# Kernel optimization log

Hardware: AMD Instinct MI355X
Metric: run time of the kernel (lower is better)

The kernel has to match this reference:

```python
import jax, jax.numpy as jnp
from jax import lax
import numpy as np

B, T, F, H, L = 64, 2048, 8, 128, 2


def _uniform(key, shape, k):
    return jax.random.uniform(key, shape, jnp.float32, -k, k)


def setup_inputs() -> dict:
    key = jax.random.key(0)
    keys = jax.random.split(key, 12)
    k = 1.0 / np.sqrt(H)
    inp = {"x": jax.random.normal(keys[0], (B, T, F), jnp.float32)}
    # layer 0: input size F; layer 1: input size H (PyTorch nn.LSTM layout: gates i,f,g,o)
    inp["w_ih0"] = _uniform(keys[1], (4 * H, F), k)
    inp["w_hh0"] = _uniform(keys[2], (4 * H, H), k)
    inp["b_ih0"] = _uniform(keys[3], (4 * H,), k)
    inp["b_hh0"] = _uniform(keys[4], (4 * H,), k)
    inp["w_ih1"] = _uniform(keys[5], (4 * H, H), k)
    inp["w_hh1"] = _uniform(keys[6], (4 * H, H), k)
    inp["b_ih1"] = _uniform(keys[7], (4 * H,), k)
    inp["b_hh1"] = _uniform(keys[8], (4 * H,), k)
    inp["w_lin"] = _uniform(keys[9], (F, H), 1.0 / np.sqrt(H))
    inp["b_lin"] = _uniform(keys[10], (F,), 1.0 / np.sqrt(H))
    return inp


def _lstm_layer(x, w_ih, w_hh, b_ih, b_hh):
    # x: [B, T, D_in]; precompute input contribution to gates: [B, T, 4H]
    xg = jnp.einsum('btd,gd->btg', x, w_ih) + b_ih + b_hh
    h0 = jnp.zeros((x.shape[0], w_hh.shape[1]), x.dtype)
    c0 = jnp.zeros_like(h0)

    def step(carry, xg_t):
        h, c = carry
        gates = xg_t + h @ w_hh.T  # [B, 4H]
        i, f, g, o = jnp.split(gates, 4, axis=-1)
        i = jax.nn.sigmoid(i)
        f = jax.nn.sigmoid(f)
        g = jnp.tanh(g)
        o = jax.nn.sigmoid(o)
        c = f * c + i * g
        h = o * jnp.tanh(c)
        return (h, c), h

    _, hs = lax.scan(step, (h0, c0), jnp.swapaxes(xg, 0, 1))  # hs: [T, B, H]
    return jnp.swapaxes(hs, 0, 1)


def reference(x, w_ih0, w_hh0, b_ih0, b_hh0, w_ih1, w_hh1, b_ih1, b_hh1, w_lin, b_lin):
    h = _lstm_layer(x, w_ih0, w_hh0, b_ih0, b_hh0)
    h = _lstm_layer(h, w_ih1, w_hh1, b_ih1, b_hh1)
    return jnp.einsum('bth,fh->btf', h, w_lin) + b_lin
```

## Files before the change

### kernel.cpp

```cpp
#include <hip/hip_runtime.h>

#define B_ 64
#define T_ 2048
#define F_ 8
#define H_ 128
#define RING_LD 68
#define CHUNK 64
#define NCH (T_ / CHUNK)
#define GRING 16
#define H0_DW (CHUNK * 64)
#define H0C_LD 68
#define Z_LD 516

typedef _Float16 v2h   __attribute__((ext_vector_type(2)));
typedef _Float16 f16x8 __attribute__((ext_vector_type(8)));
typedef float    f32x4 __attribute__((ext_vector_type(4)));

__device__ __forceinline__ unsigned pk2h(float lo, float hi) {
    v2h p;
    p[0] = (_Float16)lo;
    p[1] = (_Float16)hi;
    return __builtin_bit_cast(unsigned, p);
}

#if __has_builtin(__builtin_amdgcn_fdot2)
__device__ __forceinline__ float fdot2a(unsigned a, unsigned b, float c) {
    return __builtin_amdgcn_fdot2(__builtin_bit_cast(v2h, a),
                                  __builtin_bit_cast(v2h, b), c, false);
}
#else
__device__ __forceinline__ float fdot2a(unsigned a, unsigned b, float c) {
    v2h av = __builtin_bit_cast(v2h, a);
    v2h bv = __builtin_bit_cast(v2h, b);
    c += (float)av[0] * (float)bv[0];
    c += (float)av[1] * (float)bv[1];
    return c;
}
#endif

__device__ __forceinline__ float sigm(float x) {
    return 1.0f / (1.0f + __expf(-x));
}
__device__ __forceinline__ float tanh_f(float x) {
    float e = __expf(2.0f * x);
    return 1.0f - 2.0f / (e + 1.0f);
}

__device__ __forceinline__ f32x4 mfma16(f16x8 a, f16x8 b, f32x4 c) {
    return __builtin_amdgcn_mfma_f32_16x16x32_f16(a, b, c, 0, 0, 0);
}

#if __has_builtin(__builtin_amdgcn_mov_dpp)
template <int CTRL>
__device__ __forceinline__ float qperm(float v) {
    int i = __builtin_bit_cast(int, v);
    i = __builtin_amdgcn_mov_dpp(i, CTRL, 0xF, 0xF, true);
    return __builtin_bit_cast(float, i);
}
__device__ __forceinline__ float lane_xor1(float v) { return qperm<0xB1>(v); }
__device__ __forceinline__ float lane_xor2(float v) { return qperm<0x4E>(v); }
#else
__device__ __forceinline__ float lane_xor1(float v) {
    int i = __builtin_amdgcn_ds_swizzle(__builtin_bit_cast(int, v), 0x041F);
    return __builtin_bit_cast(float, i);
}
__device__ __forceinline__ float lane_xor2(float v) {
    int i = __builtin_amdgcn_ds_swizzle(__builtin_bit_cast(int, v), 0x081F);
    return __builtin_bit_cast(float, i);
}
#endif

__global__ __launch_bounds__(512, 2)
void lstm2_pc3_kernel(const float* __restrict__ x,
                      const float* __restrict__ wih0,
                      const float* __restrict__ whh0,
                      const float* __restrict__ bih0,
                      const float* __restrict__ bhh0,
                      const float* __restrict__ wih1,
                      const float* __restrict__ whh1,
                      const float* __restrict__ bih1,
                      const float* __restrict__ bhh1,
                      const float* __restrict__ wlin,
                      const float* __restrict__ blin,
                      unsigned* __restrict__ h0g,
                      int* __restrict__ flags,
                      float* __restrict__ out)
{
    __shared__ __align__(16) unsigned arena[25760];
    __shared__ float blin_f[F_];

    const int tid = threadIdx.x;
    int* prog = flags;
    int* done = flags + 64;

    if (blockIdx.x < 64) {
        const int b = blockIdx.x;
        unsigned* x_lds = arena;
        unsigned* ring  = arena + 8192;

        const int h_idx = tid >> 2;
        const int sub   = tid & 3;
        const int growA = (0x3120 >> (sub * 4)) & 0xF;
        const int rowA  = growA * H_ + h_idx;

        const float4* xp = (const float4*)(x + (size_t)b * T_ * F_);
        #pragma unroll
        for (int i = 0; i < 8; ++i) {
            int idx = tid + i * 512;
            float4 v = xp[idx];
            x_lds[idx * 2 + 0] = pk2h(v.x, v.y);
            x_lds[idx * 2 + 1] = pk2h(v.z, v.w);
        }

        unsigned rwih0[4];
        {
            const float4* p = (const float4*)(wih0 + (size_t)rowA * F_);
            float4 v0 = p[0], v1 = p[1];
            rwih0[0] = pk2h(v0.x, v0.y); rwih0[1] = pk2h(v0.z, v0.w);
            rwih0[2] = pk2h(v1.x, v1.y); rwih0[3] = pk2h(v1.z, v1.w);
        }
        unsigned rwhh0[64];
        {
            const float4* p = (const float4*)(whh0 + (size_t)rowA * H_);
            #pragma unroll
            for (int i = 0; i < 32; ++i) {
                float4 v = p[i];
                rwhh0[i * 2 + 0] = pk2h(v.x, v.y);
                rwhh0[i * 2 + 1] = pk2h(v.z, v.w);
            }
        }
        const float bias0 = bih0[rowA] + bhh0[rowA];

        if (tid < 64) ring[63 * 64 + tid] = 0u;
        __syncthreads();

        const bool is_g = (sub == 1);
        const bool lo2  = (sub < 2);
        float c0 = 0.0f;

        for (int t = 0; t < T_; ++t) {
            {
                float aa = bias0, ab = 0.0f, ba = 0.0f, bb = 0.0f;
                uint4 xv = *(const uint4*)&x_lds[t * 4];
                aa = fdot2a(rwih0[0], xv.x, aa);
                ab = fdot2a(rwih0[1], xv.y, ab);
                ba = fdot2a(rwih0[2], xv.z, ba);
                bb = fdot2a(rwih0[3], xv.w, bb);
                const unsigned* hr = &ring[((t + 63) & 63) * 64];
                #pragma unroll
                for (int j = 0; j < 16; ++j) {
                    uint4 hv = *(const uint4*)&hr[j * 4];
                    aa = fdot2a(rwhh0[j * 4 + 0], hv.x, aa);
                    ab = fdot2a(rwhh0[j * 4 + 1], hv.y, ab);
                    ba = fdot2a(rwhh0[j * 4 + 2], hv.z, ba);
                    bb = fdot2a(rwhh0[j * 4 + 3], hv.w, bb);
                }
                float a = (aa + ab) + (ba + bb);
                float xin = is_g ? 2.0f * a : a;
                float s   = sigm(xin);
                float act = is_g ? 2.0f * s - 1.0f : s;
                float s1  = lane_xor1(act);
                float p   = lo2 ? act * s1 : (sub == 2 ? act : s1) * c0;
                float cn  = p + lane_xor2(p);
                c0 = cn;
                float oval = (sub == 2) ? s1 : act;
                float h = oval * tanh_f(cn);
                if (sub == 2) ((_Float16*)&ring[(t & 63) * 64])[h_idx] = (_Float16)h;
            }
            __syncthreads();

            if ((t & 63) == 63) {
                const int c = t >> 6;
                if (c >= GRING) {
                    while (__hip_atomic_load(&done[b], __ATOMIC_ACQUIRE,
                                             __HIP_MEMORY_SCOPE_AGENT) < c - GRING + 1)
                        __builtin_amdgcn_s_sleep(8);
                    __syncthreads();
                }
                unsigned* dst = h0g + ((size_t)b * GRING + (c & (GRING - 1))) * H0_DW;
                uint4 v0 = *(const uint4*)&ring[tid * 8];
                uint4 v1 = *(const uint4*)&ring[tid * 8 + 4];
                *(uint4*)&dst[tid * 8]     = v0;
                *(uint4*)&dst[tid * 8 + 4] = v1;
                __syncthreads();
                if (tid == 0)
                    __hip_atomic_store(&prog[b], c + 1, __ATOMIC_RELEASE,
                                       __HIP_MEMORY_SCOPE_AGENT);
            }
        }
    } else {
        const int b = blockIdx.x - 64;
        unsigned* h0c    = arena;
        unsigned* h1ring = arena + 4352;
        float*    zih1   = (float*)(arena + 8704);
        unsigned* wlin_p = arena + 25216;

        const int w   = tid >> 6;
        const int l   = tid & 63;
        const int n   = l & 15;
        const int grp = l >> 4;

        f16x8 wih1f[4][4], whh1f[4][4];
        #pragma unroll
        for (int j = 0; j < 4; ++j) {
            const int row = j * H_ + w * 16 + n;
            #pragma unroll
            for (int s = 0; s < 4; ++s) {
                const float* p1 = wih1 + (size_t)row * H_ + s * 32 + grp * 8;
                const float* p2 = whh1 + (size_t)row * H_ + s * 32 + grp * 8;
                f16x8 f1, f2;
                #pragma unroll
                for (int jj = 0; jj < 8; ++jj) {
                    f1[jj] = (_Float16)p1[jj];
                    f2[jj] = (_Float16)p2[jj];
                }
                wih1f[j][s] = f1;
                whh1f[j][s] = f2;
            }
        }
        #pragma unroll
        for (int j = 0; j < 4; ++j)
            #pragma unroll
            for (int s = 0; s < 4; ++s) {
                asm("" : "+a"(wih1f[j][s]));
                asm("" : "+a"(whh1f[j][s]));
            }

        float bb1[4];
        #pragma unroll
        for (int j = 0; j < 4; ++j) {
            const int row = j * H_ + w * 16 + n;
            bb1[j] = bih1[row] + bhh1[row];
        }
        {
            float2 v = ((const float2*)wlin)[tid];
            wlin_p[(tid >> 6) * RING_LD + (tid & 63)] = pk2h(v.x, v.y);
        }
        if (tid < F_) blin_f[tid] = blin[tid];
        if (tid < 64) h1ring[63 * RING_LD + tid] = 0u;
        __syncthreads();

        float c1 = 0.0f;
        const f32x4 Z4 = {0.0f, 0.0f, 0.0f, 0.0f};

        for (int c = 0; c < NCH; ++c) {
            while (__hip_atomic_load(&prog[b], __ATOMIC_ACQUIRE,
                                     __HIP_MEMORY_SCOPE_AGENT) < c + 1)
                __builtin_amdgcn_s_sleep(8);
            const unsigned* src = h0g + ((size_t)b * GRING + (c & (GRING - 1))) * H0_DW;
            {
                const int tick = tid >> 3;
                const int off  = (tid & 7) * 8;
                uint4 v0 = *(const uint4*)&src[tick * 64 + off];
                uint4 v1 = *(const uint4*)&src[tick * 64 + off + 4];
                *(uint4*)&h0c[tick * H0C_LD + off]     = v0;
                *(uint4*)&h0c[tick * H0C_LD + off + 4] = v1;
            }
            __syncthreads();
            if (tid == 0)
                __hip_atomic_store(&done[b], c + 1, __ATOMIC_RELAXED,
                                   __HIP_MEMORY_SCOPE_AGENT);

            for (int half = 0; half < 2; ++half) {
                #pragma unroll
                for (int mt = 0; mt < 2; ++mt) {
                    f32x4 d0 = Z4, d1 = Z4, d2 = Z4, d3 = Z4;
                    const int trow = half * 32 + mt * 16 + n;
                    #pragma unroll
                    for (int s = 0; s < 4; ++s) {
                        f16x8 ah = __builtin_bit_cast(
                            f16x8, *(const uint4*)&h0c[trow * H0C_LD + s * 16 + grp * 4]);
                        d0 = mfma16(ah, wih1f[0][s], d0);
                        d1 = mfma16(ah, wih1f[1][s], d1);
                        d2 = mfma16(ah, wih1f[2][s], d2);
                        d3 = mfma16(ah, wih1f[3][s], d3);
                    }
                    const int zr = mt * 16 + grp * 4;
                    #pragma unroll
                    for (int reg = 0; reg < 4; ++reg) {
                        zih1[(zr + reg) * Z_LD + 0 * H_ + w * 16 + n] = d0[reg];
                        zih1[(zr + reg) * Z_LD + 1 * H_ + w * 16 + n] = d1[reg];
                        zih1[(zr + reg) * Z_LD + 2 * H_ + w * 16 + n] = d2[reg];
                        zih1[(zr + reg) * Z_LD + 3 * H_ + w * 16 + n] = d3[reg];
                    }
                }

                for (int tk = 0; tk < 32; ++tk) {
                    const int t  = c * CHUNK + half * 32 + tk;
                    const unsigned* h1r = &h1ring[((t + 63) & 63) * RING_LD];
                    f32x4 a0, a1, a2, a3;
                    {
                        f16x8 ah = __builtin_bit_cast(f16x8, *(const uint4*)&h1r[grp * 4]);
                        a0 = mfma16(ah, whh1f[0][0], Z4);
                        a1 = mfma16(ah, whh1f[1][0], Z4);
                        a2 = mfma16(ah, whh1f[2][0], Z4);
                        a3 = mfma16(ah, whh1f[3][0], Z4);
                    }
                    #pragma unroll
                    for (int s = 1; s < 4; ++s) {
                        f16x8 ah = __builtin_bit_cast(
                            f16x8, *(const uint4*)&h1r[s * 16 + grp * 4]);
                        a0 = mfma16(ah, whh1f[0][s], a0);
                        a1 = mfma16(ah, whh1f[1][s], a1);
                        a2 = mfma16(ah, whh1f[2][s], a2);
                        a3 = mfma16(ah, whh1f[3][s], a3);
                    }
                    const int zbase = (half * 32 + tk) * 0 + tk;
                    const float* zp = &zih1[(half * 32 + tk - half * 32) * Z_LD];
                    float gi = sigm(a0[0] + zp[0 * H_ + w * 16 + n] + bb1[0]);
                    float gf = sigm(a1[0] + zp[1 * H_ + w * 16 + n] + bb1[1]);
                    float gg = tanh_f(a2[0] + zp[2 * H_ + w * 16 + n] + bb1[2]);
                    float go = sigm(a3[0] + zp[3 * H_ + w * 16 + n] + bb1[3]);
                    (void)zbase;
                    c1 = gf * c1 + gi * gg;
                    float hh = go * tanh_f(c1);
                    if (l < 16)
                        ((_Float16*)&h1ring[(t & 63) * RING_LD])[w * 16 + l] = (_Float16)hh;
                    __syncthreads();
                }
            }

            {
                const int tick_i = tid >> 3;
                const int fo     = tid & 7;
                const unsigned* hp = &h1ring[tick_i * RING_LD];
                const unsigned* wv = &wlin_p[fo * RING_LD];
                float a = 0.0f;
                #pragma unroll
                for (int j = 0; j < 16; ++j) {
                    uint4 hv = *(const uint4*)&hp[j * 4];
                    uint4 wq = *(const uint4*)&wv[j * 4];
                    a = fdot2a(wq.x, hv.x, a);
                    a = fdot2a(wq.y, hv.y, a);
                    a = fdot2a(wq.z, hv.z, a);
                    a = fdot2a(wq.w, hv.w, a);
                }
                out[(size_t)b * T_ * F_ + (size_t)c * CHUNK * F_ + tid] = a + blin_f[fo];
            }
        }
    }
}

__global__ __launch_bounds__(512, 2)
void lstm2_burst_kernel(const float* __restrict__ x,
                        const float* __restrict__ wih0,
                        const float* __restrict__ whh0,
                        const float* __restrict__ bih0,
                        const float* __restrict__ bhh0,
                        const float* __restrict__ wih1,
                        const float* __restrict__ whh1,
                        const float* __restrict__ bih1,
                        const float* __restrict__ bhh1,
                        const float* __restrict__ wlin,
                        const float* __restrict__ blin,
                        float* __restrict__ out)
{
    __shared__ __align__(16) unsigned x_lds[T_ * F_ / 2];
    __shared__ __align__(16) unsigned h0_p[2][H_ / 2];
    __shared__ __align__(16) unsigned h1_ring[64 * RING_LD];
    __shared__ __align__(16) unsigned wlin_p[F_ * RING_LD];
    __shared__ float blin_f[F_];

    const int tid   = threadIdx.x;
    const int b     = blockIdx.x;
    const int h_idx = tid >> 2;
    const int sub   = tid & 3;
    const int grow  = (0x3120 >> (sub * 4)) & 0xF;
    const int row   = grow * H_ + h_idx;

    const float4* xp = (const float4*)(x + (size_t)b * T_ * F_);
    #pragma unroll
    for (int i = 0; i < 8; ++i) {
        int idx = tid + i * 512;
        float4 v = xp[idx];
        x_lds[idx * 2 + 0] = pk2h(v.x, v.y);
        x_lds[idx * 2 + 1] = pk2h(v.z, v.w);
    }

    unsigned rwih0[4];
    {
        const float4* p = (const float4*)(wih0 + (size_t)row * F_);
        float4 v0 = p[0], v1 = p[1];
        rwih0[0] = pk2h(v0.x, v0.y); rwih0[1] = pk2h(v0.z, v0.w);
        rwih0[2] = pk2h(v1.x, v1.y); rwih0[3] = pk2h(v1.z, v1.w);
    }
    unsigned rwhh0[64], rwih1[64], rwhh1[64];
    {
        const float4* p = (const float4*)(whh0 + (size_t)row * H_);
        #pragma unroll
        for (int i = 0; i < 32; ++i) {
            float4 v = p[i];
            rwhh0[i * 2 + 0] = pk2h(v.x, v.y);
            rwhh0[i * 2 + 1] = pk2h(v.z, v.w);
        }
    }
    {
        const float4* p = (const float4*)(wih1 + (size_t)row * H_);
        #pragma unroll
        for (int i = 0; i < 32; ++i) {
            float4 v = p[i];
            rwih1[i * 2 + 0] = pk2h(v.x, v.y);
            rwih1[i * 2 + 1] = pk2h(v.z, v.w);
        }
    }
    {
        const float4* p = (const float4*)(whh1 + (size_t)row * H_);
        #pragma unroll
        for (int i = 0; i < 32; ++i) {
            float4 v = p[i];
            rwhh1[i * 2 + 0] = pk2h(v.x, v.y);
            rwhh1[i * 2 + 1] = pk2h(v.z, v.w);
        }
    }
    const float bias0 = bih0[row] + bhh0[row];
    const float bias1 = bih1[row] + bhh1[row];

    {
        int r = tid >> 6, c = tid & 63;
        float2 v = ((const float2*)wlin)[r * 64 + c];
        wlin_p[r * RING_LD + c] = pk2h(v.x, v.y);
    }
    if (tid < F_) blin_f[tid] = blin[tid];
    if (tid < H_ / 2) { h0_p[0][tid] = 0u; h0_p[1][tid] = 0u; }
    if (tid < H_ / 2) h1_ring[63 * RING_LD + tid] = 0u;
    __syncthreads();

    const bool is_g = (sub == 1);
    const bool lo2  = (sub < 2);
    float c0 = 0.0f, c1 = 0.0f;

    for (int t = 0; t < T_; ++t) {
        const int rp = (t + 1) & 1;
        const int wp = t & 1;
        {
            float aa = bias0, ab = 0.0f;
            uint4 xv = *(const uint4*)&x_lds[t * 4];
            aa = fdot2a(rwih0[0], xv.x, aa);
            ab = fdot2a(rwih0[1], xv.y, ab);
            aa = fdot2a(rwih0[2], xv.z, aa);
            ab = fdot2a(rwih0[3], xv.w, ab);
            const unsigned* hr = &h0_p[rp][0];
            #pragma unroll
            for (int j = 0; j < 16; ++j) {
                uint4 hv = *(const uint4*)&hr[j * 4];
                aa = fdot2a(rwhh0[j * 4 + 0], hv.x, aa);
                ab = fdot2a(rwhh0[j * 4 + 1], hv.y, ab);
                aa = fdot2a(rwhh0[j * 4 + 2], hv.z, aa);
                ab = fdot2a(rwhh0[j * 4 + 3], hv.w, ab);
            }
            float a = aa + ab;
            float xin = is_g ? 2.0f * a : a;
            float s   = sigm(xin);
            float act = is_g ? 2.0f * s - 1.0f : s;
            float s1  = lane_xor1(act);
            float p   = lo2 ? act * s1 : (sub == 2 ? act : s1) * c0;
            float cn  = p + lane_xor2(p);
            c0 = cn;
            float oval = (sub == 2) ? s1 : act;
            float h = oval * tanh_f(cn);
            if (sub == 2) ((_Float16*)&h0_p[wp][0])[h_idx] = (_Float16)h;
        }
        __syncthreads();
        {
            float aa = bias1, ab = 0.0f, ba = 0.0f, bb = 0.0f;
            const unsigned* h0r = &h0_p[wp][0];
            const unsigned* h1r = &h1_ring[((t + 63) & 63) * RING_LD];
            #pragma unroll
            for (int j = 0; j < 16; ++j) {
                uint4 hv0 = *(const uint4*)&h0r[j * 4];
                uint4 hv1 = *(const uint4*)&h1r[j * 4];
                aa = fdot2a(rwih1[j * 4 + 0], hv0.x, aa);
                ab = fdot2a(rwih1[j * 4 + 1], hv0.y, ab);
                aa = fdot2a(rwih1[j * 4 + 2], hv0.z, aa);
                ab = fdot2a(rwih1[j * 4 + 3], hv0.w, ab);
                ba = fdot2a(rwhh1[j * 4 + 0], hv1.x, ba);
                bb = fdot2a(rwhh1[j * 4 + 1], hv1.y, bb);
                ba = fdot2a(rwhh1[j * 4 + 2], hv1.z, ba);
                bb = fdot2a(rwhh1[j * 4 + 3], hv1.w, bb);
            }
            float a = (aa + ab) + (ba + bb);
            float xin = is_g ? 2.0f * a : a;
            float s   = sigm(xin);
            float act = is_g ? 2.0f * s - 1.0f : s;
            float s1  = lane_xor1(act);
            float p   = lo2 ? act * s1 : (sub == 2 ? act : s1) * c1;
            float cn  = p + lane_xor2(p);
            c1 = cn;
            float oval = (sub == 2) ? s1 : act;
            float h = oval * tanh_f(cn);
            if (sub == 2)
                ((_Float16*)&h1_ring[(t & 63) * RING_LD])[h_idx] = (_Float16)h;
        }
        __syncthreads();
        if ((t & 63) == 63) {
            const int tick_i = tid >> 3;
            const int fo     = tid & 7;
            const unsigned* hp = &h1_ring[tick_i * RING_LD];
            const unsigned* wv = &wlin_p[fo * RING_LD];
            float a = 0.0f;
            #pragma unroll
            for (int j = 0; j < 16; ++j) {
                uint4 hv = *(const uint4*)&hp[j * 4];
                uint4 wq = *(const uint4*)&wv[j * 4];
                a = fdot2a(wq.x, hv.x, a);
                a = fdot2a(wq.y, hv.y, a);
                a = fdot2a(wq.z, hv.z, a);
                a = fdot2a(wq.w, hv.w, a);
            }
            out[(size_t)b * T_ * F_ + (size_t)(t - 63) * F_ + tid] = a + blin_f[fo];
        }
    }
}

extern "C" void kernel_launch(void* const* d_in, const int* in_sizes, int n_in,
                              void* d_out, int out_size, void* d_ws, size_t ws_size,
                              hipStream_t stream) {
    const float* x    = (const float*)d_in[0];
    const float* wih0 = (const float*)d_in[1];
    const float* whh0 = (const float*)d_in[2];
    const float* bih0 = (const float*)d_in[3];
    const float* bhh0 = (const float*)d_in[4];
    const float* wih1 = (const float*)d_in[5];
    const float* whh1 = (const float*)d_in[6];
    const float* bih1 = (const float*)d_in[7];
    const float* bhh1 = (const float*)d_in[8];
    const float* wlin = (const float*)d_in[9];
    const float* blin = (const float*)d_in[10];
    float* out = (float*)d_out;

    const size_t h0_bytes = (size_t)B_ * GRING * H0_DW * sizeof(unsigned);
    const size_t need = h0_bytes + 512;
    if (d_ws != nullptr && ws_size >= need) {
        unsigned* h0g = (unsigned*)d_ws;
        int* flags = (int*)((char*)d_ws + h0_bytes);
        hipMemsetAsync(flags, 0, 512, stream);
        lstm2_pc3_kernel<<<dim3(128), dim3(512), 0, stream>>>(
            x, wih0, whh0, bih0, bhh0, wih1, whh1, bih1, bhh1, wlin, blin,
            h0g, flags, out);
    } else {
        lstm2_burst_kernel<<<dim3(B_), dim3(512), 0, stream>>>(
            x, wih0, whh0, bih0, bhh0, wih1, whh1, bih1, bhh1, wlin, blin, out);
    }
}
```

Measured before the change: 1.495 ms.

## Move layer-0 LSTM recurrence from fdot2 dot products to MFMA per chunk

The layer-0 producer blocks drop the per-thread fdot2 gate dot products and adopt the layer-1 scheme. W_hh0 is held in f16 MFMA fragments pinned to AGPRs, and the input projection for each 16-step sub-chunk is computed with MFMA into an LDS z0 buffer. The aim is a shorter serial per-step latency on the critical recurrence, which paces the whole pipeline. The cost is four gate MFMAs per step that keep only one output column, plus an extra LDS round trip for the input projections.

```diff
diff --git a/kernel.cpp b/kernel.cpp
--- a/kernel.cpp
+++ b/kernel.cpp
@@ -9,7 +9,6 @@
 #define NCH (T_ / CHUNK)
 #define GRING 16
 #define H0_DW (CHUNK * 64)
-#define H0C_LD 68
 #define Z_LD 516
 
 typedef _Float16 v2h   __attribute__((ext_vector_type(2)));
@@ -71,7 +70,7 @@
 #endif
 
 __global__ __launch_bounds__(512, 2)
-void lstm2_pc3_kernel(const float* __restrict__ x,
+void lstm2_pc5_kernel(const float* __restrict__ x,
                       const float* __restrict__ wih0,
                       const float* __restrict__ whh0,
                       const float* __restrict__ bih0,
@@ -93,15 +92,16 @@
     int* prog = flags;
     int* done = flags + 64;
 
+    const int w   = tid >> 6;
+    const int l   = tid & 63;
+    const int n   = l & 15;
+    const int grp = l >> 4;
+
     if (blockIdx.x < 64) {
         const int b = blockIdx.x;
         unsigned* x_lds = arena;
         unsigned* ring  = arena + 8192;
-
-        const int h_idx = tid >> 2;
-        const int sub   = tid & 3;
-        const int growA = (0x3120 >> (sub * 4)) & 0xF;
-        const int rowA  = growA * H_ + h_idx;
+        float*    z0    = (float*)(arena + 12288);
 
         const float4* xp = (const float4*)(x + (size_t)b * T_ * F_);
         #pragma unroll
@@ -112,79 +112,119 @@
             x_lds[idx * 2 + 1] = pk2h(v.z, v.w);
         }
 
-        unsigned rwih0[4];
-        {
-            const float4* p = (const float4*)(wih0 + (size_t)rowA * F_);
-            float4 v0 = p[0], v1 = p[1];
-            rwih0[0] = pk2h(v0.x, v0.y); rwih0[1] = pk2h(v0.z, v0.w);
-            rwih0[2] = pk2h(v1.x, v1.y); rwih0[3] = pk2h(v1.z, v1.w);
-        }
-        unsigned rwhh0[64];
-        {
-            const float4* p = (const float4*)(whh0 + (size_t)rowA * H_);
-            #pragma unroll
-            for (int i = 0; i < 32; ++i) {
-                float4 v = p[i];
-                rwhh0[i * 2 + 0] = pk2h(v.x, v.y);
-                rwhh0[i * 2 + 1] = pk2h(v.z, v.w);
-            }
-        }
-        const float bias0 = bih0[rowA] + bhh0[rowA];
+        f16x8 whh0f[4][4];
+        #pragma unroll
+        for (int j = 0; j < 4; ++j) {
+            const int row = j * H_ + w * 16 + n;
+            #pragma unroll
+            for (int s = 0; s < 4; ++s) {
+                const float* p0 = whh0 + (size_t)row * H_ + s * 32 + grp * 8;
+                f16x8 f0;
+                #pragma unroll
+                for (int jj = 0; jj < 8; ++jj) f0[jj] = (_Float16)p0[jj];
+                whh0f[j][s] = f0;
+            }
+        }
+        #pragma unroll
+        for (int j = 0; j < 4; ++j)
+            #pragma unroll
+            for (int s = 0; s < 4; ++s)
+                asm("" : "+a"(whh0f[j][s]));
+
+        f16x8 wih0f[4];
+        #pragma unroll
+        for (int j = 0; j < 4; ++j) {
+            f16x8 f0 = {};
+            if (grp == 0) {
+                const float* p = wih0 + (size_t)(j * H_ + w * 16 + n) * F_;
+                #pragma unroll
+                for (int jj = 0; jj < 8; ++jj) f0[jj] = (_Float16)p[jj];
+            }
+            wih0f[j] = f0;
+        }
+
+        float bb0[4];
+        #pragma unroll
+        for (int j = 0; j < 4; ++j) {
+            const int row = j * H_ + w * 16 + n;
+            bb0[j] = bih0[row] + bhh0[row];
+        }
 
         if (tid < 64) ring[63 * 64 + tid] = 0u;
         __syncthreads();
 
-        const bool is_g = (sub == 1);
-        const bool lo2  = (sub < 2);
         float c0 = 0.0f;
-
-        for (int t = 0; t < T_; ++t) {
+        const f32x4 Z4 = {0.0f, 0.0f, 0.0f, 0.0f};
+
+        for (int ch = 0; ch < NCH; ++ch) {
+            for (int q = 0; q < 4; ++q) {
+                {
+                    const int tg = ch * CHUNK + q * 16 + n;
+                    f16x8 ax = (f16x8){};
+                    if (grp == 0)
+                        ax = __builtin_bit_cast(f16x8, *(const uint4*)&x_lds[tg * 4]);
+                    f32x4 d0 = mfma16(ax, wih0f[0], Z4);
+                    f32x4 d1 = mfma16(ax, wih0f[1], Z4);
+                    f32x4 d2 = mfma16(ax, wih0f[2], Z4);
+                    f32x4 d3 = mfma16(ax, wih0f[3], Z4);
+                    #pragma unroll
+                    for (int reg = 0; reg < 4; ++reg) {
+                        const int zr = (grp * 4 + reg) * Z_LD + w * 16 + n;
+                        z0[zr + 0 * H_] = d0[reg];
+                        z0[zr + 1 * H_] = d1[reg];
+                        z0[zr + 2 * H_] = d2[reg];
+                        z0[zr + 3 * H_] = d3[reg];
+                    }
+                }
+
+                for (int tk = 0; tk < 16; ++tk) {
+                    const int t = ch * CHUNK + q * 16 + tk;
+                    const unsigned* hr = &ring[((t + 63) & 63) * 64];
+                    f32x4 a0, a1, a2, a3;
+                    {
+                        f16x8 ah = __builtin_bit_cast(f16x8, *(const uint4*)&hr[grp * 4]);
+                        a0 = mfma16(ah, whh0f[0][0], Z4);
+                        a1 = mfma16(ah, whh0f[1][0], Z4);
+                        a2 = mfma16(ah, whh0f[2][0], Z4);
+                        a3 = mfma16(ah, whh0f[3][0], Z4);
+                    }
+                    #pragma unroll
+                    for (int s = 1; s < 4; ++s) {
+                        f16x8 ah = __builtin_bit_cast(
+                            f16x8, *(const uint4*)&hr[s * 16 + grp * 4]);
+                        a0 = mfma16(ah, whh0f[0][s], a0);
+                        a1 = mfma16(ah, whh0f[1][s], a1);
+                        a2 = mfma16(ah, whh0f[2][s], a2);
+                        a3 = mfma16(ah, whh0f[3][s], a3);
+                    }
+                    const float* zz = &z0[tk * Z_LD + w * 16 + n];
+                    float gi = sigm(a0[0] + zz[0 * H_] + bb0[0]);
+                    float gf = sigm(a1[0] + zz[1 * H_] + bb0[1]);
+                    float gg = tanh_f(a2[0] + zz[2 * H_] + bb0[2]);
+                    float go = sigm(a3[0] + zz[3 * H_] + bb0[3]);
+                    c0 = gf * c0 + gi * gg;
+                    float hh = go * tanh_f(c0);
+                    if (l < 16)
+                        ((_Float16*)&ring[(t & 63) * 64])[w * 16 + l] = (_Float16)hh;
+                    __syncthreads();
+                }
+            }
+
             {
-                float aa = bias0, ab = 0.0f, ba = 0.0f, bb = 0.0f;
-                uint4 xv = *(const uint4*)&x_lds[t * 4];
-                aa = fdot2a(rwih0[0], xv.x, aa);
-                ab = fdot2a(rwih0[1], xv.y, ab);
-                ba = fdot2a(rwih0[2], xv.z, ba);
-                bb = fdot2a(rwih0[3], xv.w, bb);
-                const unsigned* hr = &ring[((t + 63) & 63) * 64];
-                #pragma unroll
-                for (int j = 0; j < 16; ++j) {
-                    uint4 hv = *(const uint4*)&hr[j * 4];
-                    aa = fdot2a(rwhh0[j * 4 + 0], hv.x, aa);
-                    ab = fdot2a(rwhh0[j * 4 + 1], hv.y, ab);
-                    ba = fdot2a(rwhh0[j * 4 + 2], hv.z, ba);
-                    bb = fdot2a(rwhh0[j * 4 + 3], hv.w, bb);
-                }
-                float a = (aa + ab) + (ba + bb);
-                float xin = is_g ? 2.0f * a : a;
-                float s   = sigm(xin);
-                float act = is_g ? 2.0f * s - 1.0f : s;
-                float s1  = lane_xor1(act);
-                float p   = lo2 ? act * s1 : (sub == 2 ? act : s1) * c0;
-                float cn  = p + lane_xor2(p);
-                c0 = cn;
-                float oval = (sub == 2) ? s1 : act;
-                float h = oval * tanh_f(cn);
-                if (sub == 2) ((_Float16*)&ring[(t & 63) * 64])[h_idx] = (_Float16)h;
-            }
-            __syncthreads();
-
-            if ((t & 63) == 63) {
-                const int c = t >> 6;
-                if (c >= GRING) {
+                if (ch >= GRING) {
                     while (__hip_atomic_load(&done[b], __ATOMIC_ACQUIRE,
-                                             __HIP_MEMORY_SCOPE_AGENT) < c - GRING + 1)
+                                             __HIP_MEMORY_SCOPE_AGENT) < ch - GRING + 1)
                         __builtin_amdgcn_s_sleep(8);
                     __syncthreads();
                 }
-                unsigned* dst = h0g + ((size_t)b * GRING + (c & (GRING - 1))) * H0_DW;
+                unsigned* dst = h0g + ((size_t)b * GRING + (ch & (GRING - 1))) * H0_DW;
                 uint4 v0 = *(const uint4*)&ring[tid * 8];
                 uint4 v1 = *(const uint4*)&ring[tid * 8 + 4];
                 *(uint4*)&dst[tid * 8]     = v0;
                 *(uint4*)&dst[tid * 8 + 4] = v1;
                 __syncthreads();
                 if (tid == 0)
-                    __hip_atomic_store(&prog[b], c + 1, __ATOMIC_RELEASE,
+                    __hip_atomic_store(&prog[b], ch + 1, __ATOMIC_RELEASE,
                                        __HIP_MEMORY_SCOPE_AGENT);
             }
         }
@@ -194,11 +234,6 @@
         unsigned* h1ring = arena + 4352;
         float*    zih1   = (float*)(arena + 8704);
         unsigned* wlin_p = arena + 25216;
-
-        const int w   = tid >> 6;
-        const int l   = tid & 63;
-        const int n   = l & 15;
-        const int grp = l >> 4;
 
         f16x8 wih1f[4][4], whh1f[4][4];
         #pragma unroll
@@ -253,8 +288,8 @@
                 const int off  = (tid & 7) * 8;
                 uint4 v0 = *(const uint4*)&src[tick * 64 + off];
                 uint4 v1 = *(const uint4*)&src[tick * 64 + off + 4];
-                *(uint4*)&h0c[tick * H0C_LD + off]     = v0;
-                *(uint4*)&h0c[tick * H0C_LD + off + 4] = v1;
+                *(uint4*)&h0c[tick * RING_LD + off]     = v0;
+                *(uint4*)&h0c[tick * RING_LD + off + 4] = v1;
             }
             __syncthreads();
             if (tid == 0)
@@ -269,7 +304,7 @@
                     #pragma unroll
                     for (int s = 0; s < 4; ++s) {
                         f16x8 ah = __builtin_bit_cast(
-                            f16x8, *(const uint4*)&h0c[trow * H0C_LD + s * 16 + grp * 4]);
+                            f16x8, *(const uint4*)&h0c[trow * RING_LD + s * 16 + grp * 4]);
                         d0 = mfma16(ah, wih1f[0][s], d0);
                         d1 = mfma16(ah, wih1f[1][s], d1);
                         d2 = mfma16(ah, wih1f[2][s], d2);
@@ -305,13 +340,11 @@
                         a2 = mfma16(ah, whh1f[2][s], a2);
                         a3 = mfma16(ah, whh1f[3][s], a3);
                     }
-                    const int zbase = (half * 32 + tk) * 0 + tk;
-                    const float* zp = &zih1[(half * 32 + tk - half * 32) * Z_LD];
+                    const float* zp = &zih1[tk * Z_LD];
                     float gi = sigm(a0[0] + zp[0 * H_ + w * 16 + n] + bb1[0]);
                     float gf = sigm(a1[0] + zp[1 * H_ + w * 16 + n] + bb1[1]);
                     float gg = tanh_f(a2[0] + zp[2 * H_ + w * 16 + n] + bb1[2]);
                     float go = sigm(a3[0] + zp[3 * H_ + w * 16 + n] + bb1[3]);
-                    (void)zbase;
                     c1 = gf * c1 + gi * gg;
                     float hh = go * tanh_f(c1);
                     if (l < 16)
@@ -534,7 +567,7 @@
         unsigned* h0g = (unsigned*)d_ws;
         int* flags = (int*)((char*)d_ws + h0_bytes);
         hipMemsetAsync(flags, 0, 512, stream);
-        lstm2_pc3_kernel<<<dim3(128), dim3(512), 0, stream>>>(
+        lstm2_pc5_kernel<<<dim3(128), dim3(512), 0, stream>>>(
             x, wih0, whh0, bih0, bhh0, wih1, whh1, bih1, bhh1, wlin, blin,
             h0g, flags, out);
     } else {
```

Result: no change. 1.479 ms, median of 2 (-1.1%).
